# Kernel optimization log

Hardware: AMD Instinct MI355X
Metric: run time of the kernel (lower is better)

Reference implementation:

```python
import jax, jax.numpy as jnp
import numpy as np

B, V = 256, 2048
PD, MD, H = 1024, 512, 512

def setup_inputs() -> dict:
    key = jax.random.key(0)
    k1, k2, k3, k4, k5 = jax.random.split(key, 5)
    patient_emb = jax.random.normal(k1, (B, PD), dtype=jnp.float32)
    atc4_emb = jax.random.normal(k2, (V, MD), dtype=jnp.float32)
    # Linear(PD+MD -> H): weight (H, PD+MD), bias (H,)
    W1 = jax.random.normal(k3, (H, PD + MD), dtype=jnp.float32) * 0.02
    b1 = jnp.zeros((H,), dtype=jnp.float32)
    # Linear(H -> 1): weight (1, H) -> store as (H,), bias scalar
    w2 = jax.random.normal(k4, (H,), dtype=jnp.float32) * 0.05
    b2 = jnp.zeros((), dtype=jnp.float32)
    return {"patient_emb": patient_emb, "atc4_emb": atc4_emb,
            "W1": W1, "b1": b1, "w2": w2, "b2": b2}

def reference(patient_emb, atc4_emb, W1, b1, w2, b2):
    # Algebraically equivalent to cat([patient, mol]) @ W1.T:
    # split W1 into patient and mol blocks, matmul each, broadcast-add.
    W1p = W1[:, :PD]   # (H, PD)
    W1m = W1[:, PD:]   # (H, MD)
    hp = jnp.einsum('bp,hp->bh', patient_emb, W1p)   # (B, H)
    hm = jnp.einsum('vm,hm->vh', atc4_emb, W1m)      # (V, H)
    h = jnp.tanh(hp[:, None, :] + hm[None, :, :] + b1)  # (B, V, H)
    scores = jnp.einsum('bvh,h->bv', h, w2) + b2     # (B, V)
    return scores
```

## Files before the change

### kernel.cpp

```cpp
#include <hip/hip_runtime.h>
#include <hip/hip_bf16.h>
#include <math.h>

typedef __attribute__((ext_vector_type(8))) short short8;
typedef __attribute__((ext_vector_type(4))) short short4v;
typedef __attribute__((ext_vector_type(4))) float float4v;

__device__ __forceinline__ short f2bf(float f) {
    union { float f; unsigned u; } x; x.f = f;
    unsigned r = (x.u + 0x7FFFu + ((x.u >> 16) & 1u)) >> 16;
    return (short)r;
}

__global__ __launch_bounds__(256) void gemm_exp(
    const float* __restrict__ patient, const float* __restrict__ atc4,
    const float* __restrict__ W1, const float* __restrict__ b1,
    float* __restrict__ EA, float* __restrict__ EM)
{
    const float* A; const float* W; const float* bias; float* T;
    int lda, K, M;
    if (blockIdx.z == 0) {
        if (blockIdx.x >= 4) return;
        A = patient; lda = 1024; K = 1024; M = 256; bias = b1; T = EA; W = W1;
    } else {
        A = atc4;    lda = 512;  K = 512;  M = 2048; bias = nullptr; T = EM; W = W1 + 1024;
    }
    const int ldw = 1536;

    __shared__ short As[64][72];
    __shared__ short Bs[64][72];
    const int t = threadIdx.x;
    const int m0 = blockIdx.x * 64;
    const int n0 = blockIdx.y * 64;
    const int wave = t >> 6;
    const int lane = t & 63;
    const int wm = (wave & 1) * 32;
    const int wn = (wave >> 1) * 32;
    const int lrow = lane & 15;
    const int quad = lane >> 4;

    float4v acc[2][2];
    #pragma unroll
    for (int i = 0; i < 2; i++)
        #pragma unroll
        for (int j = 0; j < 2; j++)
            acc[i][j] = (float4v){0.f, 0.f, 0.f, 0.f};

    const int sr = t >> 2;
    const int sc = (t & 3) * 16;

    for (int k0 = 0; k0 < K; k0 += 64) {
        const float* ap = A + (size_t)(m0 + sr) * lda + (k0 + sc);
        const float* wp = W + (size_t)(n0 + sr) * ldw + (k0 + sc);
        #pragma unroll
        for (int ii = 0; ii < 4; ii++) {
            float4v av = *(const float4v*)(ap + ii * 4);
            float4v wv = *(const float4v*)(wp + ii * 4);
            short4v a4 = { f2bf(av.x), f2bf(av.y), f2bf(av.z), f2bf(av.w) };
            short4v w4 = { f2bf(wv.x), f2bf(wv.y), f2bf(wv.z), f2bf(wv.w) };
            *(short4v*)&As[sr][sc + ii * 4] = a4;
            *(short4v*)&Bs[sr][sc + ii * 4] = w4;
        }
        __syncthreads();
        #pragma unroll
        for (int kk = 0; kk < 64; kk += 32) {
            short8 af[2], bfr[2];
            #pragma unroll
            for (int i = 0; i < 2; i++)
                af[i] = *(const short8*)&As[wm + i * 16 + lrow][kk + quad * 8];
            #pragma unroll
            for (int j = 0; j < 2; j++)
                bfr[j] = *(const short8*)&Bs[wn + j * 16 + lrow][kk + quad * 8];
            #pragma unroll
            for (int i = 0; i < 2; i++)
                #pragma unroll
                for (int j = 0; j < 2; j++)
                    acc[i][j] = __builtin_amdgcn_mfma_f32_16x16x32_bf16(
                        af[i], bfr[j], acc[i][j], 0, 0, 0);
        }
        __syncthreads();
    }

    #pragma unroll
    for (int i = 0; i < 2; i++) {
        #pragma unroll
        for (int j = 0; j < 2; j++) {
            const int n  = n0 + wn + j * 16 + lrow;
            const int mb = m0 + wm + i * 16 + quad * 4;
            const float bn = bias ? bias[n] : 0.0f;
            float4v ev;
            #pragma unroll
            for (int r = 0; r < 4; r++)
                ev[r] = __expf(2.0f * (acc[i][j][r] + bn));
            *(float4v*)&T[(size_t)n * M + mb] = ev;
        }
    }
}

__global__ __launch_bounds__(256) void pair_kernel(
    const float* __restrict__ EA, const float* __restrict__ EM,
    const float* __restrict__ w2, float* __restrict__ partial)
{
    __shared__ float sEA[64][36];
    __shared__ float sEM[64][68];
    __shared__ float sC[128];
    const int t  = threadIdx.x;
    const int v0 = blockIdx.x * 64;
    const int b0 = blockIdx.y * 32;
    const int h0 = blockIdx.z * 128;
    const int tx = t & 15;
    const int ty = t >> 4;

    float w2s = 0.0f;
    for (int i = 0; i < 128; i++) w2s += w2[h0 + i];
    if (t < 128) sC[t] = -2.0f * w2[h0 + t];

    float acc[2][4];
    #pragma unroll
    for (int i = 0; i < 2; i++)
        #pragma unroll
        for (int j = 0; j < 4; j++)
            acc[i][j] = 0.0f;

    const int r  = t >> 2;
    const int cA = (t & 3) * 8;
    const int cM = (t & 3) * 16;

    for (int half = 0; half < 2; half++) {
        const int hb = h0 + half * 64;
        {
            const float* pa = EA + (size_t)(hb + r) * 256 + b0 + cA;
            *(float4v*)&sEA[r][cA]     = *(const float4v*)pa;
            *(float4v*)&sEA[r][cA + 4] = *(const float4v*)(pa + 4);
            const float* pm = EM + (size_t)(hb + r) * 2048 + v0 + cM;
            *(float4v*)&sEM[r][cM]      = *(const float4v*)pm;
            *(float4v*)&sEM[r][cM + 4]  = *(const float4v*)(pm + 4);
            *(float4v*)&sEM[r][cM + 8]  = *(const float4v*)(pm + 8);
            *(float4v*)&sEM[r][cM + 12] = *(const float4v*)(pm + 12);
        }
        __syncthreads();
        #pragma unroll 2
        for (int h = 0; h < 64; h++) {
            const float ea0 = sEA[h][ty * 2];
            const float ea1 = sEA[h][ty * 2 + 1];
            const float4v em = *(const float4v*)&sEM[h][tx * 4];
            const float c = sC[half * 64 + h];
            #pragma unroll
            for (int j = 0; j < 4; j++) {
                float d0 = __builtin_fmaf(ea0, em[j], 1.0f);
                float d1 = __builtin_fmaf(ea1, em[j], 1.0f);
                acc[0][j] = __builtin_fmaf(c, __builtin_amdgcn_rcpf(d0), acc[0][j]);
                acc[1][j] = __builtin_fmaf(c, __builtin_amdgcn_rcpf(d1), acc[1][j]);
            }
        }
        __syncthreads();
    }

    const size_t pb = (size_t)blockIdx.z * (256 * 2048);
    #pragma unroll
    for (int i = 0; i < 2; i++) {
        float4v o = { acc[i][0] + w2s, acc[i][1] + w2s, acc[i][2] + w2s, acc[i][3] + w2s };
        *(float4v*)&partial[pb + (size_t)(b0 + ty * 2 + i) * 2048 + v0 + tx * 4] = o;
    }
}

__global__ __launch_bounds__(256) void reduce_kernel(
    const float* __restrict__ partial, const float* __restrict__ b2,
    float* __restrict__ out)
{
    const int i = (blockIdx.x * 256 + threadIdx.x) * 4;
    const float bb = b2[0];
    float4v s0 = *(const float4v*)&partial[i];
    float4v s1 = *(const float4v*)&partial[524288 + i];
    float4v s2 = *(const float4v*)&partial[1048576 + i];
    float4v s3 = *(const float4v*)&partial[1572864 + i];
    float4v o = s0 + s1 + s2 + s3 + bb;
    *(float4v*)&out[i] = o;
}

extern "C" void kernel_launch(void* const* d_in, const int* in_sizes, int n_in,
                              void* d_out, int out_size, void* d_ws, size_t ws_size,
                              hipStream_t stream)
{
    const float* patient = (const float*)d_in[0];
    const float* atc4    = (const float*)d_in[1];
    const float* W1      = (const float*)d_in[2];
    const float* b1      = (const float*)d_in[3];
    const float* w2      = (const float*)d_in[4];
    const float* b2      = (const float*)d_in[5];
    float* out = (float*)d_out;
    float* ws  = (float*)d_ws;

    float* EA      = ws;
    float* EM      = ws + 131072;
    float* partial = ws + 1179648;

    gemm_exp<<<dim3(32, 8, 2), 256, 0, stream>>>(patient, atc4, W1, b1, EA, EM);
    pair_kernel<<<dim3(32, 8, 4), 256, 0, stream>>>(EA, EM, w2, partial);
    reduce_kernel<<<512, 256, 0, stream>>>(partial, b2, out);
}
```

Before: 128.3 us.

## Pair h values to share one reciprocal, and replace reduce kernel with atomics

The pair kernel now handles two hidden units per step. It combines c0/d0 + c1/d1 into a single fraction, so there is one rcp per pair instead of two, which cuts transcendental throughput by half. The EA/EM intermediates are stored interleaved by h-pair so each thread can load the paired values as vectors. The separate reduce kernel and partial buffer are removed: idle gemm blocks fill the output with b2 and the pair kernel adds its partial results with atomicAdd. The trade-offs are atomic contention, scalar strided stores in the gemm epilogue, and a possible overflow risk when the product of two denominators is formed from large exp values.

After: 133.1 us. +3.7%, slower.

```diff
diff --git a/kernel.cpp b/kernel.cpp
--- a/kernel.cpp
+++ b/kernel.cpp
@@ -5,6 +5,7 @@
 typedef __attribute__((ext_vector_type(8))) short short8;
 typedef __attribute__((ext_vector_type(4))) short short4v;
 typedef __attribute__((ext_vector_type(4))) float float4v;
+typedef __attribute__((ext_vector_type(2))) float float2v;
 
 __device__ __forceinline__ short f2bf(float f) {
     union { float f; unsigned u; } x; x.f = f;
@@ -15,15 +16,23 @@
 __global__ __launch_bounds__(256) void gemm_exp(
     const float* __restrict__ patient, const float* __restrict__ atc4,
     const float* __restrict__ W1, const float* __restrict__ b1,
-    float* __restrict__ EA, float* __restrict__ EM)
+    const float* __restrict__ b2,
+    float* __restrict__ EA2, float* __restrict__ EM2, float* __restrict__ out)
 {
     const float* A; const float* W; const float* bias; float* T;
     int lda, K, M;
     if (blockIdx.z == 0) {
-        if (blockIdx.x >= 4) return;
-        A = patient; lda = 1024; K = 1024; M = 256; bias = b1; T = EA; W = W1;
+        if (blockIdx.x >= 4) {
+            const float bb = b2[0];
+            float4v bb4 = { bb, bb, bb, bb };
+            const int fid = (blockIdx.x - 4) * 8 + blockIdx.y;
+            for (int i = fid * 256 + threadIdx.x; i < 131072; i += 224 * 256)
+                ((float4v*)out)[i] = bb4;
+            return;
+        }
+        A = patient; lda = 1024; K = 1024; M = 256; bias = b1; T = EA2; W = W1;
     } else {
-        A = atc4;    lda = 512;  K = 512;  M = 2048; bias = nullptr; T = EM; W = W1 + 1024;
+        A = atc4;    lda = 512;  K = 512;  M = 2048; bias = nullptr; T = EM2; W = W1 + 1024;
     }
     const int ldw = 1536;
 
@@ -88,22 +97,21 @@
             const int n  = n0 + wn + j * 16 + lrow;
             const int mb = m0 + wm + i * 16 + quad * 4;
             const float bn = bias ? bias[n] : 0.0f;
-            float4v ev;
+            const size_t base = (size_t)(n >> 1) * (2 * M) + (n & 1);
             #pragma unroll
             for (int r = 0; r < 4; r++)
-                ev[r] = __expf(2.0f * (acc[i][j][r] + bn));
-            *(float4v*)&T[(size_t)n * M + mb] = ev;
+                T[base + (size_t)(mb + r) * 2] = __expf(2.0f * (acc[i][j][r] + bn));
         }
     }
 }
 
 __global__ __launch_bounds__(256) void pair_kernel(
-    const float* __restrict__ EA, const float* __restrict__ EM,
-    const float* __restrict__ w2, float* __restrict__ partial)
+    const float* __restrict__ EA2, const float* __restrict__ EM2,
+    const float* __restrict__ w2, float* __restrict__ out)
 {
-    __shared__ float sEA[64][36];
-    __shared__ float sEM[64][68];
-    __shared__ float sC[128];
+    __shared__ float sEA[32][68];
+    __shared__ float sEM[32][132];
+    __shared__ float2v sC[64];
     const int t  = threadIdx.x;
     const int v0 = blockIdx.x * 64;
     const int b0 = blockIdx.y * 32;
@@ -111,9 +119,10 @@
     const int tx = t & 15;
     const int ty = t >> 4;
 
-    float w2s = 0.0f;
-    for (int i = 0; i < 128; i++) w2s += w2[h0 + i];
-    if (t < 128) sC[t] = -2.0f * w2[h0 + t];
+    if (t < 64) {
+        float2v c = { -2.0f * w2[h0 + 2 * t], -2.0f * w2[h0 + 2 * t + 1] };
+        sC[t] = c;
+    }
 
     float acc[2][4];
     #pragma unroll
@@ -122,60 +131,59 @@
         for (int j = 0; j < 4; j++)
             acc[i][j] = 0.0f;
 
-    const int r  = t >> 2;
-    const int cA = (t & 3) * 8;
-    const int cM = (t & 3) * 16;
+    const int rS = t >> 3;
+    const int cS = (t & 7) * 8;
+    const int cM = (t & 7) * 16;
 
     for (int half = 0; half < 2; half++) {
-        const int hb = h0 + half * 64;
+        const int hpb = (h0 >> 1) + half * 32;
         {
-            const float* pa = EA + (size_t)(hb + r) * 256 + b0 + cA;
-            *(float4v*)&sEA[r][cA]     = *(const float4v*)pa;
-            *(float4v*)&sEA[r][cA + 4] = *(const float4v*)(pa + 4);
-            const float* pm = EM + (size_t)(hb + r) * 2048 + v0 + cM;
-            *(float4v*)&sEM[r][cM]      = *(const float4v*)pm;
-            *(float4v*)&sEM[r][cM + 4]  = *(const float4v*)(pm + 4);
-            *(float4v*)&sEM[r][cM + 8]  = *(const float4v*)(pm + 8);
-            *(float4v*)&sEM[r][cM + 12] = *(const float4v*)(pm + 12);
+            const float* pa = EA2 + (size_t)(hpb + rS) * 512 + b0 * 2 + cS;
+            *(float4v*)&sEA[rS][cS]     = *(const float4v*)pa;
+            *(float4v*)&sEA[rS][cS + 4] = *(const float4v*)(pa + 4);
+            const float* pm = EM2 + (size_t)(hpb + rS) * 4096 + v0 * 2 + cM;
+            *(float4v*)&sEM[rS][cM]      = *(const float4v*)pm;
+            *(float4v*)&sEM[rS][cM + 4]  = *(const float4v*)(pm + 4);
+            *(float4v*)&sEM[rS][cM + 8]  = *(const float4v*)(pm + 8);
+            *(float4v*)&sEM[rS][cM + 12] = *(const float4v*)(pm + 12);
         }
         __syncthreads();
         #pragma unroll 2
-        for (int h = 0; h < 64; h++) {
-            const float ea0 = sEA[h][ty * 2];
-            const float ea1 = sEA[h][ty * 2 + 1];
-            const float4v em = *(const float4v*)&sEM[h][tx * 4];
-            const float c = sC[half * 64 + h];
-            #pragma unroll
-            for (int j = 0; j < 4; j++) {
-                float d0 = __builtin_fmaf(ea0, em[j], 1.0f);
-                float d1 = __builtin_fmaf(ea1, em[j], 1.0f);
-                acc[0][j] = __builtin_fmaf(c, __builtin_amdgcn_rcpf(d0), acc[0][j]);
-                acc[1][j] = __builtin_fmaf(c, __builtin_amdgcn_rcpf(d1), acc[1][j]);
+        for (int hp = 0; hp < 32; hp++) {
+            const float4v ea4  = *(const float4v*)&sEA[hp][ty * 4];
+            const float4v em01 = *(const float4v*)&sEM[hp][tx * 8];
+            const float4v em23 = *(const float4v*)&sEM[hp][tx * 8 + 4];
+            const float2v c = sC[half * 32 + hp];
+            float2v eaP[2] = { { ea4.x, ea4.y }, { ea4.z, ea4.w } };
+            float2v emP[4] = { { em01.x, em01.y }, { em01.z, em01.w },
+                               { em23.x, em23.y }, { em23.z, em23.w } };
+            #pragma unroll
+            for (int i = 0; i < 2; i++) {
+                #pragma unroll
+                for (int j = 0; j < 4; j++) {
+                    float2v d = __builtin_elementwise_fma(eaP[i], emP[j],
+                                                          (float2v){1.0f, 1.0f});
+                    float den = d.x * d.y;
+                    float num = __builtin_fmaf(c.x, d.y, c.y * d.x);
+                    acc[i][j] = __builtin_fmaf(num, __builtin_amdgcn_rcpf(den),
+                                               acc[i][j]);
+                }
             }
         }
         __syncthreads();
     }
 
-    const size_t pb = (size_t)blockIdx.z * (256 * 2048);
+    float w2s = 0.0f;
+    for (int k = 0; k < 64; k++) w2s += sC[k].x + sC[k].y;
+    w2s *= -0.5f;
+
     #pragma unroll
     for (int i = 0; i < 2; i++) {
-        float4v o = { acc[i][0] + w2s, acc[i][1] + w2s, acc[i][2] + w2s, acc[i][3] + w2s };
-        *(float4v*)&partial[pb + (size_t)(b0 + ty * 2 + i) * 2048 + v0 + tx * 4] = o;
-    }
-}
-
-__global__ __launch_bounds__(256) void reduce_kernel(
-    const float* __restrict__ partial, const float* __restrict__ b2,
-    float* __restrict__ out)
-{
-    const int i = (blockIdx.x * 256 + threadIdx.x) * 4;
-    const float bb = b2[0];
-    float4v s0 = *(const float4v*)&partial[i];
-    float4v s1 = *(const float4v*)&partial[524288 + i];
-    float4v s2 = *(const float4v*)&partial[1048576 + i];
-    float4v s3 = *(const float4v*)&partial[1572864 + i];
-    float4v o = s0 + s1 + s2 + s3 + bb;
-    *(float4v*)&out[i] = o;
+        const int b = b0 + ty * 2 + i;
+        #pragma unroll
+        for (int j = 0; j < 4; j++)
+            atomicAdd(&out[(size_t)b * 2048 + v0 + tx * 4 + j], acc[i][j] + w2s);
+    }
 }
 
 extern "C" void kernel_launch(void* const* d_in, const int* in_sizes, int n_in,
@@ -191,11 +199,10 @@
     float* out = (float*)d_out;
     float* ws  = (float*)d_ws;
 
-    float* EA      = ws;
-    float* EM      = ws + 131072;
-    float* partial = ws + 1179648;
-
-    gemm_exp<<<dim3(32, 8, 2), 256, 0, stream>>>(patient, atc4, W1, b1, EA, EM);
-    pair_kernel<<<dim3(32, 8, 4), 256, 0, stream>>>(EA, EM, w2, partial);
-    reduce_kernel<<<512, 256, 0, stream>>>(partial, b2, out);
-}
+    float* EA2 = ws;
+    float* EM2 = ws + 131072;
+
+    gemm_exp<<<dim3(32, 8, 2), 256, 0, stream>>>(patient, atc4, W1, b1, b2,
+                                                 EA2, EM2, out);
+    pair_kernel<<<dim3(32, 8, 4), 256, 0, stream>>>(EA2, EM2, w2, out);
+}
```

## Pair reciprocals across h to halve rcp count and prefetch second half tile

Applied to the files above, without the earlier changes.

The pair kernel's inner loop now handles two h values together and combines c_a/d_a + c_b/d_b into a single reciprocal of d_a*d_b. This halves the transcendental rcp work and uses packed float2 FMAs. It also prefetches the second 64-row half into registers while the first half is computed. The w2 sum is now built from shared memory instead of 128 global loads per thread. Multiplying the denominators risks overflow, because the exp values can be large, which could produce inf or NaN.

New measurement: 129.1 us. About the same (+0.6%).

```diff
diff --git a/kernel.cpp b/kernel.cpp
--- a/kernel.cpp
+++ b/kernel.cpp
@@ -5,6 +5,7 @@
 typedef __attribute__((ext_vector_type(8))) short short8;
 typedef __attribute__((ext_vector_type(4))) short short4v;
 typedef __attribute__((ext_vector_type(4))) float float4v;
+typedef __attribute__((ext_vector_type(2))) float float2v;
 
 __device__ __forceinline__ short f2bf(float f) {
     union { float f; unsigned u; } x; x.f = f;
@@ -103,7 +104,7 @@
 {
     __shared__ float sEA[64][36];
     __shared__ float sEM[64][68];
-    __shared__ float sC[128];
+    __shared__ float2v sC[64];
     const int t  = threadIdx.x;
     const int v0 = blockIdx.x * 64;
     const int b0 = blockIdx.y * 32;
@@ -111,9 +112,10 @@
     const int tx = t & 15;
     const int ty = t >> 4;
 
-    float w2s = 0.0f;
-    for (int i = 0; i < 128; i++) w2s += w2[h0 + i];
-    if (t < 128) sC[t] = -2.0f * w2[h0 + t];
+    if (t < 64) {
+        float2v c = { -2.0f * w2[h0 + 2 * t], -2.0f * w2[h0 + 2 * t + 1] };
+        sC[t] = c;
+    }
 
     float acc[2][4];
     #pragma unroll
@@ -122,44 +124,73 @@
         for (int j = 0; j < 4; j++)
             acc[i][j] = 0.0f;
 
-    const int r  = t >> 2;
+    const int rS = t >> 2;
     const int cA = (t & 3) * 8;
     const int cM = (t & 3) * 16;
 
+    float4v pA0, pA1, pM0, pM1, pM2, pM3;
+    {
+        const float* pa = EA + (size_t)(h0 + rS) * 256 + b0 + cA;
+        pA0 = *(const float4v*)pa;  pA1 = *(const float4v*)(pa + 4);
+        const float* pm = EM + (size_t)(h0 + rS) * 2048 + v0 + cM;
+        pM0 = *(const float4v*)pm;      pM1 = *(const float4v*)(pm + 4);
+        pM2 = *(const float4v*)(pm + 8); pM3 = *(const float4v*)(pm + 12);
+    }
+    *(float4v*)&sEA[rS][cA]      = pA0;  *(float4v*)&sEA[rS][cA + 4]  = pA1;
+    *(float4v*)&sEM[rS][cM]      = pM0;  *(float4v*)&sEM[rS][cM + 4]  = pM1;
+    *(float4v*)&sEM[rS][cM + 8]  = pM2;  *(float4v*)&sEM[rS][cM + 12] = pM3;
+    __syncthreads();
+    {
+        const float* pa = EA + (size_t)(h0 + 64 + rS) * 256 + b0 + cA;
+        pA0 = *(const float4v*)pa;  pA1 = *(const float4v*)(pa + 4);
+        const float* pm = EM + (size_t)(h0 + 64 + rS) * 2048 + v0 + cM;
+        pM0 = *(const float4v*)pm;      pM1 = *(const float4v*)(pm + 4);
+        pM2 = *(const float4v*)(pm + 8); pM3 = *(const float4v*)(pm + 12);
+    }
+
+    #pragma unroll
     for (int half = 0; half < 2; half++) {
-        const int hb = h0 + half * 64;
-        {
-            const float* pa = EA + (size_t)(hb + r) * 256 + b0 + cA;
-            *(float4v*)&sEA[r][cA]     = *(const float4v*)pa;
-            *(float4v*)&sEA[r][cA + 4] = *(const float4v*)(pa + 4);
-            const float* pm = EM + (size_t)(hb + r) * 2048 + v0 + cM;
-            *(float4v*)&sEM[r][cM]      = *(const float4v*)pm;
-            *(float4v*)&sEM[r][cM + 4]  = *(const float4v*)(pm + 4);
-            *(float4v*)&sEM[r][cM + 8]  = *(const float4v*)(pm + 8);
-            *(float4v*)&sEM[r][cM + 12] = *(const float4v*)(pm + 12);
-        }
-        __syncthreads();
         #pragma unroll 2
-        for (int h = 0; h < 64; h++) {
-            const float ea0 = sEA[h][ty * 2];
-            const float ea1 = sEA[h][ty * 2 + 1];
-            const float4v em = *(const float4v*)&sEM[h][tx * 4];
-            const float c = sC[half * 64 + h];
+        for (int hp = 0; hp < 32; hp++) {
+            const int ha = 2 * hp, hb = 2 * hp + 1;
+            float2v eaP[2];
+            eaP[0] = (float2v){ sEA[ha][ty * 2],     sEA[hb][ty * 2]     };
+            eaP[1] = (float2v){ sEA[ha][ty * 2 + 1], sEA[hb][ty * 2 + 1] };
+            const float4v em0 = *(const float4v*)&sEM[ha][tx * 4];
+            const float4v em1 = *(const float4v*)&sEM[hb][tx * 4];
+            const float2v c = sC[half * 32 + hp];
             #pragma unroll
             for (int j = 0; j < 4; j++) {
-                float d0 = __builtin_fmaf(ea0, em[j], 1.0f);
-                float d1 = __builtin_fmaf(ea1, em[j], 1.0f);
-                acc[0][j] = __builtin_fmaf(c, __builtin_amdgcn_rcpf(d0), acc[0][j]);
-                acc[1][j] = __builtin_fmaf(c, __builtin_amdgcn_rcpf(d1), acc[1][j]);
+                const float2v em = { em0[j], em1[j] };
+                #pragma unroll
+                for (int i = 0; i < 2; i++) {
+                    float2v d = __builtin_elementwise_fma(eaP[i], em,
+                                                          (float2v){1.0f, 1.0f});
+                    float den = d.x * d.y;
+                    float num = __builtin_fmaf(c.x, d.y, c.y * d.x);
+                    acc[i][j] = __builtin_fmaf(num, __builtin_amdgcn_rcpf(den),
+                                               acc[i][j]);
+                }
             }
         }
-        __syncthreads();
-    }
+        if (half == 0) {
+            __syncthreads();
+            *(float4v*)&sEA[rS][cA]      = pA0;  *(float4v*)&sEA[rS][cA + 4]  = pA1;
+            *(float4v*)&sEM[rS][cM]      = pM0;  *(float4v*)&sEM[rS][cM + 4]  = pM1;
+            *(float4v*)&sEM[rS][cM + 8]  = pM2;  *(float4v*)&sEM[rS][cM + 12] = pM3;
+            __syncthreads();
+        }
+    }
+
+    float w2s = 0.0f;
+    for (int k = 0; k < 64; k++) w2s += sC[k].x + sC[k].y;
+    w2s *= -0.5f;
 
     const size_t pb = (size_t)blockIdx.z * (256 * 2048);
     #pragma unroll
     for (int i = 0; i < 2; i++) {
-        float4v o = { acc[i][0] + w2s, acc[i][1] + w2s, acc[i][2] + w2s, acc[i][3] + w2s };
+        float4v o = { acc[i][0] + w2s, acc[i][1] + w2s,
+                      acc[i][2] + w2s, acc[i][3] + w2s };
         *(float4v*)&partial[pb + (size_t)(b0 + ty * 2 + i) * 2048 + v0 + tx * 4] = o;
     }
 }
```

## Pair reciprocals algebraically and split H dimension finer with register prefetch

Applied to the files above, without the earlier changes.

Combines two tanh terms c0/d0 + c1/d1 into a single fraction so each pair of hidden units needs one reciprocal instead of two, vectorising the arithmetic. The H reduction is split across 8 blocks instead of 4 with smaller shared tiles, higher occupancy bounds, and a register prefetch of the second tile. The extra split doubles the partial buffer and reduce traffic, and the product of denominators risks overflow for large exponentials.

New measurement: 121.8 us. -5.1%, faster.

```diff
diff --git a/kernel.cpp b/kernel.cpp
--- a/kernel.cpp
+++ b/kernel.cpp
@@ -5,6 +5,7 @@
 typedef __attribute__((ext_vector_type(8))) short short8;
 typedef __attribute__((ext_vector_type(4))) short short4v;
 typedef __attribute__((ext_vector_type(4))) float float4v;
+typedef __attribute__((ext_vector_type(2))) float float2v;
 
 __device__ __forceinline__ short f2bf(float f) {
     union { float f; unsigned u; } x; x.f = f;
@@ -97,69 +98,92 @@
     }
 }
 
-__global__ __launch_bounds__(256) void pair_kernel(
+__global__ __launch_bounds__(256, 8) void pair_kernel(
     const float* __restrict__ EA, const float* __restrict__ EM,
     const float* __restrict__ w2, float* __restrict__ partial)
 {
-    __shared__ float sEA[64][36];
-    __shared__ float sEM[64][68];
-    __shared__ float sC[128];
+    __shared__ float sEA[32][36];
+    __shared__ float sEM[32][68];
+    __shared__ float2v sC[32];
     const int t  = threadIdx.x;
     const int v0 = blockIdx.x * 64;
     const int b0 = blockIdx.y * 32;
-    const int h0 = blockIdx.z * 128;
+    const int h0 = blockIdx.z * 64;
     const int tx = t & 15;
     const int ty = t >> 4;
 
-    float w2s = 0.0f;
-    for (int i = 0; i < 128; i++) w2s += w2[h0 + i];
-    if (t < 128) sC[t] = -2.0f * w2[h0 + t];
-
-    float acc[2][4];
-    #pragma unroll
-    for (int i = 0; i < 2; i++)
-        #pragma unroll
-        for (int j = 0; j < 4; j++)
-            acc[i][j] = 0.0f;
-
-    const int r  = t >> 2;
-    const int cA = (t & 3) * 8;
-    const int cM = (t & 3) * 16;
-
+    if (t < 32) {
+        float2v c = { -2.0f * w2[h0 + 2 * t], -2.0f * w2[h0 + 2 * t + 1] };
+        sC[t] = c;
+    }
+
+    float4v acc[2];
+    acc[0] = (float4v){0.f, 0.f, 0.f, 0.f};
+    acc[1] = (float4v){0.f, 0.f, 0.f, 0.f};
+    const float4v one4 = {1.f, 1.f, 1.f, 1.f};
+
+    const int rS = t >> 3;
+    const int cA = (t & 7) * 4;
+    const int cM = (t & 7) * 8;
+
+    float4v pA, pM0, pM1;
+    {
+        pA  = *(const float4v*)(EA + (size_t)(h0 + rS) * 256 + b0 + cA);
+        const float* pm = EM + (size_t)(h0 + rS) * 2048 + v0 + cM;
+        pM0 = *(const float4v*)pm;  pM1 = *(const float4v*)(pm + 4);
+    }
+    *(float4v*)&sEA[rS][cA] = pA;
+    *(float4v*)&sEM[rS][cM] = pM0;  *(float4v*)&sEM[rS][cM + 4] = pM1;
+    __syncthreads();
+    {
+        pA  = *(const float4v*)(EA + (size_t)(h0 + 32 + rS) * 256 + b0 + cA);
+        const float* pm = EM + (size_t)(h0 + 32 + rS) * 2048 + v0 + cM;
+        pM0 = *(const float4v*)pm;  pM1 = *(const float4v*)(pm + 4);
+    }
+
+    #pragma unroll
     for (int half = 0; half < 2; half++) {
-        const int hb = h0 + half * 64;
-        {
-            const float* pa = EA + (size_t)(hb + r) * 256 + b0 + cA;
-            *(float4v*)&sEA[r][cA]     = *(const float4v*)pa;
-            *(float4v*)&sEA[r][cA + 4] = *(const float4v*)(pa + 4);
-            const float* pm = EM + (size_t)(hb + r) * 2048 + v0 + cM;
-            *(float4v*)&sEM[r][cM]      = *(const float4v*)pm;
-            *(float4v*)&sEM[r][cM + 4]  = *(const float4v*)(pm + 4);
-            *(float4v*)&sEM[r][cM + 8]  = *(const float4v*)(pm + 8);
-            *(float4v*)&sEM[r][cM + 12] = *(const float4v*)(pm + 12);
-        }
-        __syncthreads();
         #pragma unroll 2
-        for (int h = 0; h < 64; h++) {
-            const float ea0 = sEA[h][ty * 2];
-            const float ea1 = sEA[h][ty * 2 + 1];
-            const float4v em = *(const float4v*)&sEM[h][tx * 4];
-            const float c = sC[half * 64 + h];
-            #pragma unroll
-            for (int j = 0; j < 4; j++) {
-                float d0 = __builtin_fmaf(ea0, em[j], 1.0f);
-                float d1 = __builtin_fmaf(ea1, em[j], 1.0f);
-                acc[0][j] = __builtin_fmaf(c, __builtin_amdgcn_rcpf(d0), acc[0][j]);
-                acc[1][j] = __builtin_fmaf(c, __builtin_amdgcn_rcpf(d1), acc[1][j]);
+        for (int hp = 0; hp < 16; hp++) {
+            const int ha = 2 * hp, hb = 2 * hp + 1;
+            const float4v em0 = *(const float4v*)&sEM[ha][tx * 4];
+            const float4v em1 = *(const float4v*)&sEM[hb][tx * 4];
+            const float2v c = sC[half * 16 + hp];
+            const float4v c0 = { c.x, c.x, c.x, c.x };
+            const float4v c1 = { c.y, c.y, c.y, c.y };
+            #pragma unroll
+            for (int i = 0; i < 2; i++) {
+                const float ea0 = sEA[ha][ty * 2 + i];
+                const float ea1 = sEA[hb][ty * 2 + i];
+                const float4v ea0v = { ea0, ea0, ea0, ea0 };
+                const float4v ea1v = { ea1, ea1, ea1, ea1 };
+                float4v d0  = __builtin_elementwise_fma(em0, ea0v, one4);
+                float4v d1  = __builtin_elementwise_fma(em1, ea1v, one4);
+                float4v den = d0 * d1;
+                float4v num = __builtin_elementwise_fma(d1, c0, d0 * c1);
+                float4v r = { __builtin_amdgcn_rcpf(den.x),
+                              __builtin_amdgcn_rcpf(den.y),
+                              __builtin_amdgcn_rcpf(den.z),
+                              __builtin_amdgcn_rcpf(den.w) };
+                acc[i] = __builtin_elementwise_fma(num, r, acc[i]);
             }
         }
-        __syncthreads();
-    }
+        if (half == 0) {
+            __syncthreads();
+            *(float4v*)&sEA[rS][cA] = pA;
+            *(float4v*)&sEM[rS][cM] = pM0;  *(float4v*)&sEM[rS][cM + 4] = pM1;
+            __syncthreads();
+        }
+    }
+
+    float2v w2p = sC[0];
+    for (int k = 1; k < 32; k++) w2p += sC[k];
+    const float w2s = -0.5f * (w2p.x + w2p.y);
 
     const size_t pb = (size_t)blockIdx.z * (256 * 2048);
     #pragma unroll
     for (int i = 0; i < 2; i++) {
-        float4v o = { acc[i][0] + w2s, acc[i][1] + w2s, acc[i][2] + w2s, acc[i][3] + w2s };
+        float4v o = acc[i] + w2s;
         *(float4v*)&partial[pb + (size_t)(b0 + ty * 2 + i) * 2048 + v0 + tx * 4] = o;
     }
 }
@@ -170,11 +194,11 @@
 {
     const int i = (blockIdx.x * 256 + threadIdx.x) * 4;
     const float bb = b2[0];
-    float4v s0 = *(const float4v*)&partial[i];
-    float4v s1 = *(const float4v*)&partial[524288 + i];
-    float4v s2 = *(const float4v*)&partial[1048576 + i];
-    float4v s3 = *(const float4v*)&partial[1572864 + i];
-    float4v o = s0 + s1 + s2 + s3 + bb;
+    float4v s = *(const float4v*)&partial[i];
+    #pragma unroll
+    for (int z = 1; z < 8; z++)
+        s += *(const float4v*)&partial[(size_t)z * 524288 + i];
+    float4v o = s + bb;
     *(float4v*)&out[i] = o;
 }
 
@@ -196,6 +220,6 @@
     float* partial = ws + 1179648;
 
     gemm_exp<<<dim3(32, 8, 2), 256, 0, stream>>>(patient, atc4, W1, b1, EA, EM);
-    pair_kernel<<<dim3(32, 8, 4), 256, 0, stream>>>(EA, EM, w2, partial);
+    pair_kernel<<<dim3(32, 8, 8), 256, 0, stream>>>(EA, EM, w2, partial);
     reduce_kernel<<<512, 256, 0, stream>>>(partial, b2, out);
 }
```
